# Kernel optimization log

Measured on AMD Instinct MI355X. Metric: run time of the kernel, lower is better.

## Reference

```python
import jax, jax.numpy as jnp
import numpy as np

N, E, HID, H_SA, H_MHA, L = 20000, 320000, 128, 4, 4, 32
MLP_HID = 4 * HID
EPS = 1e-6


def _ln(x, eps=EPS):
    mu = jnp.mean(x, axis=-1, keepdims=True)
    var = jnp.var(x, axis=-1, keepdims=True)
    return (x - mu) * jax.lax.rsqrt(var + eps)


def _modulate(x, shift, scale):
    return x * (1.0 + scale) + shift


def setup_inputs() -> dict:
    key = jax.random.key(0)
    ks = jax.random.split(key, 32)
    s = 0.02
    inp = {
        'x': jax.random.normal(ks[0], (N, HID), jnp.float32),
        'edge_index': jax.random.randint(ks[1], (2, E), 0, N, jnp.int64),
        't': jax.random.normal(ks[2], (N, HID), jnp.float32),
        'text_emb': jax.random.normal(ks[3], (N, L, HID), jnp.float32),
        # TransformerConv (per-head out_channels = HID, concat=False)
        'sa_q_w': jax.random.normal(ks[4], (HID, H_SA * HID), jnp.float32) * s,
        'sa_q_b': jnp.zeros((H_SA * HID,), jnp.float32),
        'sa_k_w': jax.random.normal(ks[5], (HID, H_SA * HID), jnp.float32) * s,
        'sa_k_b': jnp.zeros((H_SA * HID,), jnp.float32),
        'sa_v_w': jax.random.normal(ks[6], (HID, H_SA * HID), jnp.float32) * s,
        'sa_v_b': jnp.zeros((H_SA * HID,), jnp.float32),
        'sa_skip_w': jax.random.normal(ks[7], (HID, HID), jnp.float32) * s,
        'sa_skip_b': jnp.zeros((HID,), jnp.float32),
        # norm3 affine
        'n3_g': jnp.ones((HID,), jnp.float32),
        'n3_b': jnp.zeros((HID,), jnp.float32),
        # MultiheadAttention
        'mha_q_w': jax.random.normal(ks[8], (HID, HID), jnp.float32) * s,
        'mha_q_b': jnp.zeros((HID,), jnp.float32),
        'mha_k_w': jax.random.normal(ks[9], (HID, HID), jnp.float32) * s,
        'mha_k_b': jnp.zeros((HID,), jnp.float32),
        'mha_v_w': jax.random.normal(ks[10], (HID, HID), jnp.float32) * s,
        'mha_v_b': jnp.zeros((HID,), jnp.float32),
        'mha_o_w': jax.random.normal(ks[11], (HID, HID), jnp.float32) * s,
        'mha_o_b': jnp.zeros((HID,), jnp.float32),
        # MLP
        'fc1_w': jax.random.normal(ks[12], (HID, MLP_HID), jnp.float32) * s,
        'fc1_b': jnp.zeros((MLP_HID,), jnp.float32),
        'fc2_w': jax.random.normal(ks[13], (MLP_HID, HID), jnp.float32) * s,
        'fc2_b': jnp.zeros((HID,), jnp.float32),
        # adaLN modulation
        'ada_w': jax.random.normal(ks[14], (HID, 6 * HID), jnp.float32) * s,
        'ada_b': jnp.zeros((6 * HID,), jnp.float32),
    }
    return inp


def reference(x, edge_index, t, text_emb,
              sa_q_w, sa_q_b, sa_k_w, sa_k_b, sa_v_w, sa_v_b, sa_skip_w, sa_skip_b,
              n3_g, n3_b,
              mha_q_w, mha_q_b, mha_k_w, mha_k_b, mha_v_w, mha_v_b, mha_o_w, mha_o_b,
              fc1_w, fc1_b, fc2_w, fc2_b, ada_w, ada_b):
    n = x.shape[0]
    # adaLN: SiLU -> Linear -> chunk(6)
    mod = jax.nn.silu(t) @ ada_w + ada_b  # [N, 6*HID]
    shift_msa, scale_msa, gate_msa, shift_mlp, scale_mlp, gate_mlp = jnp.split(mod, 6, axis=1)

    # ---- graph self-attention (PyG TransformerConv, concat=False) ----
    xm = _modulate(_ln(x), shift_msa, scale_msa)  # [N, HID]
    q = (xm @ sa_q_w + sa_q_b).reshape(n, H_SA, HID)
    k = (xm @ sa_k_w + sa_k_b).reshape(n, H_SA, HID)
    v = (xm @ sa_v_w + sa_v_b).reshape(n, H_SA, HID)
    src, dst = edge_index[0], edge_index[1]  # messages flow src -> dst
    # per-edge attention logits [E, H]
    logits = jnp.einsum('ehd,ehd->eh', q[dst], k[src]) / jnp.sqrt(jnp.float32(HID))
    m = jax.ops.segment_max(logits, dst, num_segments=n)          # [N, H]
    ex = jnp.exp(logits - m[dst])                                  # [E, H]
    den = jax.ops.segment_sum(ex, dst, num_segments=n)            # [N, H]
    alpha = ex / den[dst]                                          # [E, H]
    agg = jax.ops.segment_sum(alpha[:, :, None] * v[src], dst, num_segments=n)  # [N, H, HID]
    sa_out = agg.mean(axis=1) + (xm @ sa_skip_w + sa_skip_b)       # concat=False -> head mean, + root skip
    x = x + gate_msa * sa_out

    # ---- cross attention: each node attends over its text memory ----
    qn = _ln(x) * n3_g + n3_b                                      # norm3 (affine)
    dh = HID // H_MHA
    qh = (qn @ mha_q_w + mha_q_b).reshape(n, H_MHA, dh)
    kh = (text_emb @ mha_k_w + mha_k_b).reshape(n, L, H_MHA, dh)
    vh = (text_emb @ mha_v_w + mha_v_b).reshape(n, L, H_MHA, dh)
    scores = jnp.einsum('nhd,nlhd->nhl', qh, kh) / jnp.sqrt(jnp.float32(dh))
    attn = jax.nn.softmax(scores, axis=-1)
    ctx = jnp.einsum('nhl,nlhd->nhd', attn, vh).reshape(n, HID)
    x = x + (ctx @ mha_o_w + mha_o_b)

    # ---- gated MLP ----
    xm2 = _modulate(_ln(x), shift_mlp, scale_mlp)
    h = jax.nn.gelu(xm2 @ fc1_w + fc1_b, approximate=True)
    x = x + gate_mlp * (h @ fc2_w + fc2_b)
    return x
```

## Files before the change

### kernel.cpp

```cpp
#include <hip/hip_runtime.h>
#include <hip/hip_bf16.h>
#include <math.h>

using ushort8 = __attribute__((ext_vector_type(8))) unsigned short;
using short8  = __attribute__((ext_vector_type(8))) short;
using f32x4   = __attribute__((ext_vector_type(4))) float;
using f32x2   = __attribute__((ext_vector_type(2))) float;

__device__ __forceinline__ float bf2f(unsigned short u) {
    union { unsigned int i; float f; } c; c.i = ((unsigned int)u) << 16; return c.f;
}
__device__ __forceinline__ unsigned short f2bf(float f) {
    __hip_bfloat16 h = __float2bfloat16(f);
    return *reinterpret_cast<unsigned short*>(&h);
}
__device__ __forceinline__ float silu_f(float x) { return x / (1.f + __expf(-x)); }
__device__ __forceinline__ float gelu_f(float x) {
    float x3 = x * x * x;
    return 0.5f * x * (1.f + tanhf(0.7978845608028654f * (x + 0.044715f * x3)));
}

constexpr int QKV_STRIDE_B = 2304;

template<int WM, int AIN, int PRE, int EPI, int OUTBF>
__global__ __launch_bounds__(256) void gemm_mfma(
    const void* __restrict__ Ain, const unsigned short* __restrict__ Wt,
    const float* __restrict__ bias, void* __restrict__ Cout,
    const float* __restrict__ res, const void* __restrict__ gatep,
    int Nrows, int K, int M)
{
    constexpr int BM = 32 * WM;
    __shared__ unsigned short As[BM][64];
    __shared__ unsigned short Bs[128][64];
    const int tid = threadIdx.x;
    const int row0 = blockIdx.x * BM;
    const int col0 = blockIdx.y * 128;
    const int lane = tid & 63;
    const int wid  = tid >> 6;
    const int wr = (wid >> 1) * 16 * WM;
    const int wc = (wid & 1) * 64;
    const int lr = lane & 15;
    const int lk = lane >> 4;

    f32x4 acc[WM][4];
#pragma unroll
    for (int i = 0; i < WM; i++)
#pragma unroll
        for (int j = 0; j < 4; j++) acc[i][j] = (f32x4)0.f;

    for (int k0 = 0; k0 < K; k0 += 64) {
#pragma unroll
        for (int i = 0; i < BM * 8 / 256; i++) {
            int f = tid + i * 256;
            int m = f >> 3, b = f & 7;
            int r = row0 + m;
            ushort8 h;
            if (r < Nrows) {
                if (AIN == 1) {
                    h = *(const ushort8*)((const unsigned short*)Ain + (size_t)r * K + k0 + b * 8);
                } else {
                    const float* ap = (const float*)Ain + (size_t)r * K + k0 + b * 8;
                    float4 p0 = *(const float4*)ap;
                    float4 p1 = *(const float4*)(ap + 4);
                    float v[8] = {p0.x, p0.y, p0.z, p0.w, p1.x, p1.y, p1.z, p1.w};
                    if (PRE == 1) {
#pragma unroll
                        for (int j = 0; j < 8; j++) v[j] = silu_f(v[j]);
                    }
#pragma unroll
                    for (int j = 0; j < 8; j++) h[j] = f2bf(v[j]);
                }
            } else {
#pragma unroll
                for (int j = 0; j < 8; j++) h[j] = 0;
            }
            *(ushort8*)&As[m][((b ^ (m & 7))) * 8] = h;
        }
#pragma unroll
        for (int i = 0; i < 4; i++) {
            int f = tid + i * 256;
            int n = f >> 3, b = f & 7;
            ushort8 w = *(const ushort8*)(Wt + (size_t)(col0 + n) * K + k0 + b * 8);
            *(ushort8*)&Bs[n][((b ^ (n & 7))) * 8] = w;
        }
        __syncthreads();

        short8 afr[WM][2], bfr[4][2];
#pragma unroll
        for (int fr = 0; fr < WM; fr++)
#pragma unroll
            for (int s = 0; s < 2; s++) {
                int m = wr + fr * 16 + lr;
                int blk = (s * 4 + lk) ^ (m & 7);
                afr[fr][s] = *(const short8*)&As[m][blk * 8];
            }
#pragma unroll
        for (int fc = 0; fc < 4; fc++)
#pragma unroll
            for (int s = 0; s < 2; s++) {
                int n = wc + fc * 16 + lr;
                int blk = (s * 4 + lk) ^ (n & 7);
                bfr[fc][s] = *(const short8*)&Bs[n][blk * 8];
            }
#pragma unroll
        for (int fr = 0; fr < WM; fr++)
#pragma unroll
            for (int fc = 0; fc < 4; fc++)
#pragma unroll
                for (int s = 0; s < 2; s++)
                    acc[fr][fc] = __builtin_amdgcn_mfma_f32_16x16x32_bf16(
                        afr[fr][s], bfr[fc][s], acc[fr][fc], 0, 0, 0);
        __syncthreads();
    }

#pragma unroll
    for (int fr = 0; fr < WM; fr++) {
#pragma unroll
        for (int fc = 0; fc < 4; fc++) {
#pragma unroll
            for (int r = 0; r < 4; r++) {
                int row = row0 + wr + fr * 16 + (lane >> 4) * 4 + r;
                if (row >= Nrows) continue;
                int col = col0 + wc + fc * 16 + (lane & 15);
                float val = acc[fr][fc][r] + bias[col];
                if (EPI == 4) {
                    unsigned char* rowp = (unsigned char*)Cout + (size_t)row * QKV_STRIDE_B;
                    if (col < 512) {
                        *(unsigned short*)(rowp + 2 * col) = f2bf(val);
                    } else if (col < 1536) {
                        int p = __builtin_amdgcn_cvt_pk_fp8_f32(val, 0.f, 0, false);
                        rowp[1024 + (col - 512)] = (unsigned char)(p & 0xff);
                    } else {
                        *(unsigned short*)(rowp + 2048 + 2 * (col - 1536)) = f2bf(val);
                    }
                } else {
                    size_t idx = (size_t)row * M + col;
                    if (EPI == 1) val = gelu_f(val);
                    else if (EPI == 2) val = res[idx] + val;
                    else if (EPI == 3) val = res[idx] +
                        bf2f(((const unsigned short*)gatep)[(size_t)row * 768 + col]) * val;
                    if (OUTBF) ((unsigned short*)Cout)[idx] = f2bf(val);
                    else       ((float*)Cout)[idx] = val;
                }
            }
        }
    }
}

__global__ __launch_bounds__(256) void conv_all(
    const float* __restrict__ qW, const float* __restrict__ qB,
    const float* __restrict__ kW, const float* __restrict__ kB,
    const float* __restrict__ vW, const float* __restrict__ vB,
    const float* __restrict__ sW, const float* __restrict__ sB,
    const float* __restrict__ f1W, const float* __restrict__ f2W,
    const float* __restrict__ adW,
    unsigned short* __restrict__ Wsa_t, float* __restrict__ bsa,
    unsigned short* __restrict__ fc1_t, unsigned short* __restrict__ fc2_t,
    unsigned short* __restrict__ ada_t)
{
    int g = blockIdx.x * 256 + threadIdx.x;
    if (g < 65536) {
        int m = g >> 7, kk = g & 127;
        Wsa_t[m * 128 + kk] = f2bf(qW[(size_t)kk * 512 + m]);
        if (kk == 0) bsa[m] = qB[m];
    } else if (g < 131072) {
        int l = g - 65536; int m = l >> 7, kk = l & 127;
        int p = 512 + ((m >> 2) << 3) + (m & 3);
        Wsa_t[p * 128 + kk] = f2bf(kW[(size_t)kk * 512 + m]);
        if (kk == 0) bsa[p] = kB[m];
    } else if (g < 196608) {
        int l = g - 131072; int m = l >> 7, kk = l & 127;
        int p = 516 + ((m >> 2) << 3) + (m & 3);
        Wsa_t[p * 128 + kk] = f2bf(vW[(size_t)kk * 512 + m]);
        if (kk == 0) bsa[p] = vB[m];
    } else if (g < 212992) {
        int l = g - 196608; int m = l >> 7, kk = l & 127;
        Wsa_t[(1536 + m) * 128 + kk] = f2bf(sW[(size_t)kk * 128 + m]);
        if (kk == 0) bsa[1536 + m] = sB[m];
    } else if (g < 278528) {
        int l = g - 212992; int m = l >> 7, kk = l & 127;
        fc1_t[m * 128 + kk] = f2bf(f1W[(size_t)kk * 512 + m]);
    } else if (g < 344064) {
        int l = g - 278528; int m = l >> 9, kk = l & 511;
        fc2_t[m * 512 + kk] = f2bf(f2W[(size_t)kk * 128 + m]);
    } else if (g < 442368) {
        int l = g - 344064; int m = l >> 7, kk = l & 127;
        ada_t[m * 128 + kk] = f2bf(adW[(size_t)kk * 768 + m]);
    }
}

__global__ __launch_bounds__(256) void prep_weights(
    const float* __restrict__ Wq, const float* __restrict__ bq,
    const float* __restrict__ Wk, const float* __restrict__ Wv,
    const float* __restrict__ bv, const float* __restrict__ Wo,
    const float* __restrict__ bo,
    unsigned short* __restrict__ Mcat_t, float* __restrict__ biasM,
    unsigned short* __restrict__ Pcat_t, float* __restrict__ co)
{
    int g = blockIdx.x * 256 + threadIdx.x;
    {
        int i0 = g >> 9, col = g & 511, h = col >> 7, i = col & 127;
        float s = 0.f;
#pragma unroll 8
        for (int j = 0; j < 32; j++)
            s += Wq[i0 * 128 + h * 32 + j] * Wk[i * 128 + h * 32 + j];
        Mcat_t[col * 128 + i0] = f2bf(s);
    }
    {
        int rowp = g >> 7, j = g & 127, h = rowp >> 7, i = rowp & 127;
        float s = 0.f;
#pragma unroll 8
        for (int d = 0; d < 32; d++)
            s += Wv[i * 128 + h * 32 + d] * Wo[(h * 32 + d) * 128 + j];
        Pcat_t[j * 512 + rowp] = f2bf(s);
    }
    if (g < 512) {
        int h = g >> 7, i = g & 127;
        float s = 0.f;
        for (int j = 0; j < 32; j++)
            s += bq[h * 32 + j] * Wk[i * 128 + h * 32 + j];
        biasM[g] = s;
    }
    if (g < 128) {
        float s = bo[g];
        for (int m = 0; m < 128; m++) s += bv[m] * Wo[m * 128 + g];
        co[g] = s;
    }
}

__global__ __launch_bounds__(256) void ln_mod_kernel(
    const float* __restrict__ x, const unsigned short* __restrict__ mod,
    int shift_off, int scale_off, unsigned short* __restrict__ outb, int N)
{
    int node = blockIdx.x * 4 + (threadIdx.x >> 6);
    if (node >= N) return;
    int lane = threadIdx.x & 63;
    f32x2 v = *(const f32x2*)(x + (size_t)node * 128 + lane * 2);
    float s = v[0] + v[1], ss = v[0] * v[0] + v[1] * v[1];
#pragma unroll
    for (int m = 1; m < 64; m <<= 1) { s += __shfl_xor(s, m); ss += __shfl_xor(ss, m); }
    float mu = s * (1.f / 128.f);
    float rs = rsqrtf(ss * (1.f / 128.f) - mu * mu + 1e-6f);
    const unsigned short* mp = mod + (size_t)node * 768;
    ushort2 sh = *(const ushort2*)(mp + shift_off + lane * 2);
    ushort2 sc = *(const ushort2*)(mp + scale_off + lane * 2);
    ushort2 o;
    o.x = f2bf((v[0] - mu) * rs * (1.f + bf2f(sc.x)) + bf2f(sh.x));
    o.y = f2bf((v[1] - mu) * rs * (1.f + bf2f(sc.y)) + bf2f(sh.y));
    *(ushort2*)(outb + (size_t)node * 128 + lane * 2) = o;
}

__global__ void count_edges(const int* __restrict__ dst, int* __restrict__ count, int E) {
    int e = blockIdx.x * blockDim.x + threadIdx.x;
    if (e < E) atomicAdd(&count[dst[e]], 1);
}

__global__ __launch_bounds__(1024) void scan_block(const int* __restrict__ cnt,
                                                   int* __restrict__ pre,
                                                   int* __restrict__ bsum, int n)
{
    __shared__ int tmp[1024];
    int gid = blockIdx.x * 1024 + threadIdx.x;
    int v = (gid < n) ? cnt[gid] : 0;
    tmp[threadIdx.x] = v;
    __syncthreads();
    for (int off = 1; off < 1024; off <<= 1) {
        int add = (threadIdx.x >= off) ? tmp[threadIdx.x - off] : 0;
        __syncthreads();
        tmp[threadIdx.x] += add;
        __syncthreads();
    }
    if (gid < n) pre[gid] = tmp[threadIdx.x];
    if (threadIdx.x == 1023) bsum[blockIdx.x] = tmp[1023];
}

__global__ void scan_tops(int* __restrict__ bsum, int nb) {
    if (threadIdx.x == 0 && blockIdx.x == 0) {
        int c = 0;
        for (int i = 0; i < nb; i++) { int v = bsum[i]; bsum[i] = c; c += v; }
    }
}

__global__ void scan_fix(const int* __restrict__ pre, const int* __restrict__ bsum,
                         const int* __restrict__ cnt,
                         int* __restrict__ base, int* __restrict__ cursor, int n)
{
    int gid = blockIdx.x * 256 + threadIdx.x;
    if (gid < n) {
        int inc = pre[gid] + bsum[gid >> 10];
        base[gid + 1] = inc;
        cursor[gid] = inc - cnt[gid];
    }
    if (gid == 0) base[0] = 0;
}

__global__ void scatter_edges(const int* __restrict__ src, const int* __restrict__ dst,
                              int* __restrict__ cursor, int* __restrict__ csr_src, int E) {
    int e = blockIdx.x * blockDim.x + threadIdx.x;
    if (e < E) {
        int pos = atomicAdd(&cursor[dst[e]], 1);
        csr_src[pos] = src[e];
    }
}

__global__ __launch_bounds__(128) void sa_node_kernel(
    const unsigned char* __restrict__ qkv,
    const int* __restrict__ base, const int* __restrict__ csr_src,
    const float* __restrict__ x, const unsigned short* __restrict__ mod,
    const float* __restrict__ n3g, const float* __restrict__ n3b,
    float* __restrict__ x1, unsigned short* __restrict__ qn)
{
    int node = blockIdx.x, t = threadIdx.x;
    const unsigned char* nrow = qkv + (size_t)node * QKV_STRIDE_B;
    ushort4 qu = *(const ushort4*)((const unsigned short*)nrow + t * 4);
    const float sc = 0.08838834764831845f;
    float q0 = bf2f(qu.x) * sc, q1 = bf2f(qu.y) * sc;
    float q2 = bf2f(qu.z) * sc, q3 = bf2f(qu.w) * sc;
    int beg = base[node], end = base[node + 1];
    float den = 0.f, a0 = 0.f, a1 = 0.f, a2 = 0.f, a3 = 0.f;
    uint2 kva = make_uint2(0, 0), kvb = make_uint2(0, 0);
    if (beg < end)
        kva = *(const uint2*)(qkv + (size_t)csr_src[beg] * QKV_STRIDE_B + 1024 + t * 8);
    if (beg + 1 < end)
        kvb = *(const uint2*)(qkv + (size_t)csr_src[beg + 1] * QKV_STRIDE_B + 1024 + t * 8);
    for (int e = beg; e < end; e++) {
        uint2 cur = kva;
        kva = kvb;
        if (e + 2 < end)
            kvb = *(const uint2*)(qkv + (size_t)csr_src[e + 2] * QKV_STRIDE_B + 1024 + t * 8);
        f32x2 k01 = __builtin_amdgcn_cvt_pk_f32_fp8(cur.x, false);
        f32x2 k23 = __builtin_amdgcn_cvt_pk_f32_fp8(cur.x, true);
        f32x2 v01 = __builtin_amdgcn_cvt_pk_f32_fp8(cur.y, false);
        f32x2 v23 = __builtin_amdgcn_cvt_pk_f32_fp8(cur.y, true);
        float p = q0 * k01[0] + q1 * k01[1] + q2 * k23[0] + q3 * k23[1];
#pragma unroll
        for (int mm = 1; mm < 32; mm <<= 1) p += __shfl_xor(p, mm);
        float pe = __expf(fminf(p, 80.f));
        den += pe;
        a0 += pe * v01[0];
        a1 += pe * v01[1];
        a2 += pe * v23[0];
        a3 += pe * v23[1];
    }
    float inv = (den > 0.f) ? 0.25f / den : 0.f;
    __shared__ float red[512];
    *(float4*)&red[t * 4] = make_float4(a0 * inv, a1 * inv, a2 * inv, a3 * inv);
    __syncthreads();
    float sa = red[t] + red[128 + t] + red[256 + t] + red[384 + t];
    float sab = bf2f(*(const unsigned short*)(nrow + 2048 + 2 * t));
    float g = bf2f(mod[(size_t)node * 768 + 256 + t]);
    size_t idx = (size_t)node * 128 + t;
    float xv = x[idx] + g * (sa + sab);
    x1[idx] = xv;
    float s = xv, ssq = xv * xv;
#pragma unroll
    for (int m = 1; m < 64; m <<= 1) { s += __shfl_xor(s, m); ssq += __shfl_xor(ssq, m); }
    __shared__ float l_s[2], l_ss[2];
    int w = t >> 6;
    if ((t & 63) == 0) { l_s[w] = s; l_ss[w] = ssq; }
    __syncthreads();
    float S = l_s[0] + l_s[1], SS = l_ss[0] + l_ss[1];
    float mu = S * (1.f / 128.f);
    float rs = rsqrtf(SS * (1.f / 128.f) - mu * mu + 1e-6f);
    qn[idx] = f2bf((xv - mu) * rs * n3g[t] + n3b[t]);
}

__global__ __launch_bounds__(128) void cross_mid_kernel(
    const float* __restrict__ te, const unsigned short* __restrict__ qw,
    unsigned short* __restrict__ u)
{
    int node = blockIdx.x, t = threadIdx.x;
    __shared__ float tes[32 * 132];
    __shared__ float qws[512];
    __shared__ float attnL[128];
#pragma unroll
    for (int i = 0; i < 8; i++) {
        int f = t + i * 128;
        int l = f >> 5, ii = (f & 31) * 4;
        float4 val = *(const float4*)(te + (size_t)node * 4096 + l * 128 + ii);
        *(float4*)&tes[l * 132 + ii] = val;
    }
    {
        ushort4 qv = *(const ushort4*)(qw + (size_t)node * 512 + t * 4);
        qws[t * 4 + 0] = bf2f(qv.x);
        qws[t * 4 + 1] = bf2f(qv.y);
        qws[t * 4 + 2] = bf2f(qv.z);
        qws[t * 4 + 3] = bf2f(qv.w);
    }
    __syncthreads();

    int h = t >> 5, l = t & 31;
    float sc = 0.f;
#pragma unroll 8
    for (int i = 0; i < 128; i++) sc += tes[l * 132 + i] * qws[h * 128 + i];
    sc *= 0.17677669529663687f;
    float mx = sc;
#pragma unroll
    for (int mm = 1; mm < 32; mm <<= 1) mx = fmaxf(mx, __shfl_xor(mx, mm));
    float e = __expf(sc - mx);
    float ssum = e;
#pragma unroll
    for (int mm = 1; mm < 32; mm <<= 1) ssum += __shfl_xor(ssum, mm);
    attnL[t] = e / ssum;
    __syncthreads();

    int i0 = t & 31;
    float u0 = 0, u1 = 0, u2 = 0, u3 = 0;
#pragma unroll 4
    for (int ll = 0; ll < 32; ll++) {
        float a = attnL[h * 32 + ll];
        u0 += a * tes[ll * 132 + i0];
        u1 += a * tes[ll * 132 + i0 + 32];
        u2 += a * tes[ll * 132 + i0 + 64];
        u3 += a * tes[ll * 132 + i0 + 96];
    }
    size_t ub = (size_t)node * 512 + h * 128;
    u[ub + i0] = f2bf(u0);
    u[ub + i0 + 32] = f2bf(u1);
    u[ub + i0 + 64] = f2bf(u2);
    u[ub + i0 + 96] = f2bf(u3);
}

extern "C" void kernel_launch(void* const* d_in, const int* in_sizes, int n_in,
                              void* d_out, int out_size, void* d_ws, size_t ws_size,
                              hipStream_t stream)
{
    const int N = in_sizes[0] / 128;
    const int E = in_sizes[1] / 2;

    const float* x      = (const float*)d_in[0];
    const int*   ei     = (const int*)d_in[1];
    const float* t_in   = (const float*)d_in[2];
    const float* te     = (const float*)d_in[3];
    const float* sa_q_w = (const float*)d_in[4];
    const float* sa_q_b = (const float*)d_in[5];
    const float* sa_k_w = (const float*)d_in[6];
    const float* sa_k_b = (const float*)d_in[7];
    const float* sa_v_w = (const float*)d_in[8];
    const float* sa_v_b = (const float*)d_in[9];
    const float* sa_skip_w = (const float*)d_in[10];
    const float* sa_skip_b = (const float*)d_in[11];
    const float* n3_g   = (const float*)d_in[12];
    const float* n3_b   = (const float*)d_in[13];
    const float* mha_q_w = (const float*)d_in[14];
    const float* mha_q_b = (const float*)d_in[15];
    const float* mha_k_w = (const float*)d_in[16];
    const float* mha_v_w = (const float*)d_in[18];
    const float* mha_v_b = (const float*)d_in[19];
    const float* mha_o_w = (const float*)d_in[20];
    const float* mha_o_b = (const float*)d_in[21];
    const float* fc1_w  = (const float*)d_in[22];
    const float* fc1_b  = (const float*)d_in[23];
    const float* fc2_w  = (const float*)d_in[24];
    const float* fc2_b  = (const float*)d_in[25];
    const float* ada_w  = (const float*)d_in[26];
    const float* ada_b  = (const float*)d_in[27];
    float* out = (float*)d_out;

    float* ws = (float*)d_ws;
    size_t o = 0;
    unsigned short* modb = (unsigned short*)(ws + o); o += (size_t)N * 384;
    unsigned short* Bbuf = (unsigned short*)(ws + o); o += (size_t)N * 64;
    unsigned short* Qn   = (unsigned short*)(ws + o); o += (size_t)N * 64;
    unsigned short* Cbuf = (unsigned short*)(ws + o); o += (size_t)N * 256;
    unsigned short* Dbuf = (unsigned short*)(ws + o); o += (size_t)N * 256;
    unsigned short* Ebuf = (unsigned short*)(ws + o); o += (size_t)N * 256;
    float* Gbuf = ws + o; o += (size_t)N * 128;
    unsigned char* QKV = (unsigned char*)(ws + o); o += (size_t)N * (QKV_STRIDE_B / 4);
    unsigned short* Wsa_t  = (unsigned short*)(ws + o); o += 1664 * 128 / 2;
    unsigned short* Mcat_t = (unsigned short*)(ws + o); o += 512 * 128 / 2;
    unsigned short* Pcat_t = (unsigned short*)(ws + o); o += 128 * 512 / 2;
    unsigned short* fc1_t  = (unsigned short*)(ws + o); o += 512 * 128 / 2;
    unsigned short* fc2_t  = (unsigned short*)(ws + o); o += 128 * 512 / 2;
    unsigned short* ada_t  = (unsigned short*)(ws + o); o += 768 * 128 / 2;
    float* bsa   = ws + o; o += 1664;
    float* biasM = ws + o; o += 512;
    float* co    = ws + o; o += 128;
    int* count   = (int*)(ws + o); o += N;
    int* base    = (int*)(ws + o); o += N + 4;
    int* cursor  = (int*)(ws + o); o += N;
    int* pre     = (int*)(ws + o); o += N;
    int* bsum    = (int*)(ws + o); o += 32;
    int* csr_src = (int*)(ws + o); o += E;

    const int* src = ei;
    const int* dst = ei + E;
    const int rb128 = (N + 127) / 128;
    const int rb64  = (N + 63) / 64;
    const int nScan = (N + 1023) / 1024;

    conv_all<<<1728, 256, 0, stream>>>(sa_q_w, sa_q_b, sa_k_w, sa_k_b,
                                       sa_v_w, sa_v_b, sa_skip_w, sa_skip_b,
                                       fc1_w, fc2_w, ada_w,
                                       Wsa_t, bsa, fc1_t, fc2_t, ada_t);
    prep_weights<<<256, 256, 0, stream>>>(mha_q_w, mha_q_b, mha_k_w, mha_v_w,
                                          mha_v_b, mha_o_w, mha_o_b,
                                          Mcat_t, biasM, Pcat_t, co);

    hipMemsetAsync(count, 0, (size_t)N * sizeof(int), stream);
    count_edges<<<(E + 255) / 256, 256, 0, stream>>>(dst, count, E);
    scan_block<<<nScan, 1024, 0, stream>>>(count, pre, bsum, N);
    scan_tops<<<1, 64, 0, stream>>>(bsum, nScan);
    scan_fix<<<(N + 255) / 256, 256, 0, stream>>>(pre, bsum, count, base, cursor, N);
    scatter_edges<<<(E + 255) / 256, 256, 0, stream>>>(src, dst, cursor, csr_src, E);

    gemm_mfma<4, 0, 1, 0, 1><<<dim3(rb128, 6), 256, 0, stream>>>(
        t_in, ada_t, ada_b, modb, nullptr, nullptr, N, 128, 768);

    ln_mod_kernel<<<(N + 3) / 4, 256, 0, stream>>>(x, modb, 0, 128, Bbuf, N);

    gemm_mfma<4, 1, 0, 4, 1><<<dim3(rb128, 13), 256, 0, stream>>>(
        Bbuf, Wsa_t, bsa, QKV, nullptr, nullptr, N, 128, 1664);

    sa_node_kernel<<<N, 128, 0, stream>>>(QKV, base, csr_src, x, modb,
                                          n3_g, n3_b, Gbuf, Qn);

    gemm_mfma<4, 1, 0, 0, 1><<<dim3(rb128, 4), 256, 0, stream>>>(
        Qn, Mcat_t, biasM, Cbuf, nullptr, nullptr, N, 128, 512);
    cross_mid_kernel<<<N, 128, 0, stream>>>(te, Cbuf, Dbuf);
    gemm_mfma<2, 1, 0, 2, 0><<<dim3(rb64, 1), 256, 0, stream>>>(
        Dbuf, Pcat_t, co, Gbuf, Gbuf, nullptr, N, 512, 128);

    ln_mod_kernel<<<(N + 3) / 4, 256, 0, stream>>>(Gbuf, modb, 384, 512, Bbuf, N);
    gemm_mfma<4, 1, 0, 1, 1><<<dim3(rb128, 4), 256, 0, stream>>>(
        Bbuf, fc1_t, fc1_b, Ebuf, nullptr, nullptr, N, 128, 512);
    gemm_mfma<2, 1, 0, 3, 0><<<dim3(rb64, 1), 256, 0, stream>>>(
        Ebuf, fc2_t, fc2_b, out, Gbuf, modb + 640, N, 512, 128);
}
```

Before: 382.6 us.

## Fuse LayerNorm-modulate into K=128 GEMMs with single-stage full-K tiles

Adds a KF=1 GEMM path that loads the whole K=128 slab into shared memory in one pass. In PRE=2 mode it computes LayerNorm plus adaLN shift/scale inside the A-tile load, which removes the two ln_mod_kernel launches and their bf16 round-trip buffer. The SA edge loop is also unrolled by two, with dual accumulators and deeper prefetch. The cost is a larger LDS footprint for these GEMMs and redundant LN statistics recomputed by every column block (13 blocks for QKV, 4 for fc1).

```diff
diff --git a/kernel.cpp b/kernel.cpp
--- a/kernel.cpp
+++ b/kernel.cpp
@@ -22,16 +22,18 @@
 
 constexpr int QKV_STRIDE_B = 2304;
 
-template<int WM, int AIN, int PRE, int EPI, int OUTBF>
+template<int WM, int KF, int AIN, int PRE, int EPI, int OUTBF>
 __global__ __launch_bounds__(256) void gemm_mfma(
     const void* __restrict__ Ain, const unsigned short* __restrict__ Wt,
     const float* __restrict__ bias, void* __restrict__ Cout,
     const float* __restrict__ res, const void* __restrict__ gatep,
+    const unsigned short* __restrict__ mod, int shift_off, int scale_off,
     int Nrows, int K, int M)
 {
     constexpr int BM = 32 * WM;
-    __shared__ unsigned short As[BM][64];
-    __shared__ unsigned short Bs[128][64];
+    constexpr int KW = KF ? 128 : 64;
+    __shared__ unsigned short As[BM][KW];
+    __shared__ unsigned short Bs[128][KW];
     const int tid = threadIdx.x;
     const int row0 = blockIdx.x * BM;
     const int col0 = blockIdx.y * 128;
@@ -48,18 +50,55 @@
 #pragma unroll
         for (int j = 0; j < 4; j++) acc[i][j] = (f32x4)0.f;
 
-    for (int k0 = 0; k0 < K; k0 += 64) {
-#pragma unroll
-        for (int i = 0; i < BM * 8 / 256; i++) {
+    if (KF == 1) {
+#pragma unroll
+        for (int i = 0; i < BM * 16 / 256; i++) {
             int f = tid + i * 256;
-            int m = f >> 3, b = f & 7;
+            int m = f >> 4, b = f & 15;
             int r = row0 + m;
             ushort8 h;
-            if (r < Nrows) {
-                if (AIN == 1) {
-                    h = *(const ushort8*)((const unsigned short*)Ain + (size_t)r * K + k0 + b * 8);
+            if (PRE == 2) {
+                float v[8];
+                if (r < Nrows) {
+                    const float* ap = (const float*)Ain + (size_t)r * 128 + b * 8;
+                    float4 p0 = *(const float4*)ap;
+                    float4 p1 = *(const float4*)(ap + 4);
+                    v[0]=p0.x; v[1]=p0.y; v[2]=p0.z; v[3]=p0.w;
+                    v[4]=p1.x; v[5]=p1.y; v[6]=p1.z; v[7]=p1.w;
                 } else {
-                    const float* ap = (const float*)Ain + (size_t)r * K + k0 + b * 8;
+#pragma unroll
+                    for (int j = 0; j < 8; j++) v[j] = 0.f;
+                }
+                float s = 0.f, ss = 0.f;
+#pragma unroll
+                for (int j = 0; j < 8; j++) { s += v[j]; ss += v[j] * v[j]; }
+#pragma unroll
+                for (int mm = 1; mm < 16; mm <<= 1) {
+                    s += __shfl_xor(s, mm); ss += __shfl_xor(ss, mm);
+                }
+                float mu = s * (1.f / 128.f);
+                float rs = rsqrtf(ss * (1.f / 128.f) - mu * mu + 1e-6f);
+                if (r < Nrows) {
+                    const unsigned short* mp = mod + (size_t)r * 768;
+                    ushort8 shv = *(const ushort8*)(mp + shift_off + b * 8);
+                    ushort8 scv = *(const ushort8*)(mp + scale_off + b * 8);
+#pragma unroll
+                    for (int j = 0; j < 8; j++)
+                        h[j] = f2bf((v[j] - mu) * rs * (1.f + bf2f(scv[j])) + bf2f(shv[j]));
+                } else {
+#pragma unroll
+                    for (int j = 0; j < 8; j++) h[j] = 0;
+                }
+            } else if (AIN == 1) {
+                if (r < Nrows)
+                    h = *(const ushort8*)((const unsigned short*)Ain + (size_t)r * 128 + b * 8);
+                else {
+#pragma unroll
+                    for (int j = 0; j < 8; j++) h[j] = 0;
+                }
+            } else {
+                if (r < Nrows) {
+                    const float* ap = (const float*)Ain + (size_t)r * 128 + b * 8;
                     float4 p0 = *(const float4*)ap;
                     float4 p1 = *(const float4*)(ap + 4);
                     float v[8] = {p0.x, p0.y, p0.z, p0.w, p1.x, p1.y, p1.z, p1.w};
@@ -69,48 +108,95 @@
                     }
 #pragma unroll
                     for (int j = 0; j < 8; j++) h[j] = f2bf(v[j]);
-                }
-            } else {
-#pragma unroll
-                for (int j = 0; j < 8; j++) h[j] = 0;
+                } else {
+#pragma unroll
+                    for (int j = 0; j < 8; j++) h[j] = 0;
+                }
             }
             *(ushort8*)&As[m][((b ^ (m & 7))) * 8] = h;
         }
 #pragma unroll
-        for (int i = 0; i < 4; i++) {
+        for (int i = 0; i < 8; i++) {
             int f = tid + i * 256;
-            int n = f >> 3, b = f & 7;
-            ushort8 w = *(const ushort8*)(Wt + (size_t)(col0 + n) * K + k0 + b * 8);
+            int n = f >> 4, b = f & 15;
+            ushort8 w = *(const ushort8*)(Wt + (size_t)(col0 + n) * 128 + b * 8);
             *(ushort8*)&Bs[n][((b ^ (n & 7))) * 8] = w;
         }
         __syncthreads();
-
-        short8 afr[WM][2], bfr[4][2];
-#pragma unroll
-        for (int fr = 0; fr < WM; fr++)
-#pragma unroll
-            for (int s = 0; s < 2; s++) {
+#pragma unroll
+        for (int s = 0; s < 4; s++) {
+            short8 afr[WM], bfr[4];
+#pragma unroll
+            for (int fr = 0; fr < WM; fr++) {
                 int m = wr + fr * 16 + lr;
                 int blk = (s * 4 + lk) ^ (m & 7);
-                afr[fr][s] = *(const short8*)&As[m][blk * 8];
+                afr[fr] = *(const short8*)&As[m][blk * 8];
             }
 #pragma unroll
-        for (int fc = 0; fc < 4; fc++)
-#pragma unroll
-            for (int s = 0; s < 2; s++) {
+            for (int fc = 0; fc < 4; fc++) {
                 int n = wc + fc * 16 + lr;
                 int blk = (s * 4 + lk) ^ (n & 7);
-                bfr[fc][s] = *(const short8*)&Bs[n][blk * 8];
+                bfr[fc] = *(const short8*)&Bs[n][blk * 8];
             }
 #pragma unroll
-        for (int fr = 0; fr < WM; fr++)
+            for (int fr = 0; fr < WM; fr++)
+#pragma unroll
+                for (int fc = 0; fc < 4; fc++)
+                    acc[fr][fc] = __builtin_amdgcn_mfma_f32_16x16x32_bf16(
+                        afr[fr], bfr[fc], acc[fr][fc], 0, 0, 0);
+        }
+    } else {
+        for (int k0 = 0; k0 < K; k0 += 64) {
+#pragma unroll
+            for (int i = 0; i < BM * 8 / 256; i++) {
+                int f = tid + i * 256;
+                int m = f >> 3, b = f & 7;
+                int r = row0 + m;
+                ushort8 h;
+                if (r < Nrows) {
+                    h = *(const ushort8*)((const unsigned short*)Ain + (size_t)r * K + k0 + b * 8);
+                } else {
+#pragma unroll
+                    for (int j = 0; j < 8; j++) h[j] = 0;
+                }
+                *(ushort8*)&As[m][((b ^ (m & 7))) * 8] = h;
+            }
+#pragma unroll
+            for (int i = 0; i < 4; i++) {
+                int f = tid + i * 256;
+                int n = f >> 3, b = f & 7;
+                ushort8 w = *(const ushort8*)(Wt + (size_t)(col0 + n) * K + k0 + b * 8);
+                *(ushort8*)&Bs[n][((b ^ (n & 7))) * 8] = w;
+            }
+            __syncthreads();
+
+            short8 afr[WM][2], bfr[4][2];
+#pragma unroll
+            for (int fr = 0; fr < WM; fr++)
+#pragma unroll
+                for (int s = 0; s < 2; s++) {
+                    int m = wr + fr * 16 + lr;
+                    int blk = (s * 4 + lk) ^ (m & 7);
+                    afr[fr][s] = *(const short8*)&As[m][blk * 8];
+                }
 #pragma unroll
             for (int fc = 0; fc < 4; fc++)
 #pragma unroll
-                for (int s = 0; s < 2; s++)
-                    acc[fr][fc] = __builtin_amdgcn_mfma_f32_16x16x32_bf16(
-                        afr[fr][s], bfr[fc][s], acc[fr][fc], 0, 0, 0);
-        __syncthreads();
+                for (int s = 0; s < 2; s++) {
+                    int n = wc + fc * 16 + lr;
+                    int blk = (s * 4 + lk) ^ (n & 7);
+                    bfr[fc][s] = *(const short8*)&Bs[n][blk * 8];
+                }
+#pragma unroll
+            for (int fr = 0; fr < WM; fr++)
+#pragma unroll
+                for (int fc = 0; fc < 4; fc++)
+#pragma unroll
+                    for (int s = 0; s < 2; s++)
+                        acc[fr][fc] = __builtin_amdgcn_mfma_f32_16x16x32_bf16(
+                            afr[fr][s], bfr[fc][s], acc[fr][fc], 0, 0, 0);
+            __syncthreads();
+        }
     }
 
 #pragma unroll
@@ -228,28 +314,6 @@
     }
 }
 
-__global__ __launch_bounds__(256) void ln_mod_kernel(
-    const float* __restrict__ x, const unsigned short* __restrict__ mod,
-    int shift_off, int scale_off, unsigned short* __restrict__ outb, int N)
-{
-    int node = blockIdx.x * 4 + (threadIdx.x >> 6);
-    if (node >= N) return;
-    int lane = threadIdx.x & 63;
-    f32x2 v = *(const f32x2*)(x + (size_t)node * 128 + lane * 2);
-    float s = v[0] + v[1], ss = v[0] * v[0] + v[1] * v[1];
-#pragma unroll
-    for (int m = 1; m < 64; m <<= 1) { s += __shfl_xor(s, m); ss += __shfl_xor(ss, m); }
-    float mu = s * (1.f / 128.f);
-    float rs = rsqrtf(ss * (1.f / 128.f) - mu * mu + 1e-6f);
-    const unsigned short* mp = mod + (size_t)node * 768;
-    ushort2 sh = *(const ushort2*)(mp + shift_off + lane * 2);
-    ushort2 sc = *(const ushort2*)(mp + scale_off + lane * 2);
-    ushort2 o;
-    o.x = f2bf((v[0] - mu) * rs * (1.f + bf2f(sc.x)) + bf2f(sh.x));
-    o.y = f2bf((v[1] - mu) * rs * (1.f + bf2f(sc.y)) + bf2f(sh.y));
-    *(ushort2*)(outb + (size_t)node * 128 + lane * 2) = o;
-}
-
 __global__ void count_edges(const int* __restrict__ dst, int* __restrict__ count, int E) {
     int e = blockIdx.x * blockDim.x + threadIdx.x;
     if (e < E) atomicAdd(&count[dst[e]], 1);
@@ -317,31 +381,45 @@
     float q0 = bf2f(qu.x) * sc, q1 = bf2f(qu.y) * sc;
     float q2 = bf2f(qu.z) * sc, q3 = bf2f(qu.w) * sc;
     int beg = base[node], end = base[node + 1];
-    float den = 0.f, a0 = 0.f, a1 = 0.f, a2 = 0.f, a3 = 0.f;
-    uint2 kva = make_uint2(0, 0), kvb = make_uint2(0, 0);
+    float den0 = 0.f, a00 = 0.f, a01 = 0.f, a02 = 0.f, a03 = 0.f;
+    float den1 = 0.f, a10 = 0.f, a11 = 0.f, a12 = 0.f, a13 = 0.f;
+    uint2 c0 = make_uint2(0, 0), c1 = make_uint2(0, 0);
     if (beg < end)
-        kva = *(const uint2*)(qkv + (size_t)csr_src[beg] * QKV_STRIDE_B + 1024 + t * 8);
+        c0 = *(const uint2*)(qkv + (size_t)csr_src[beg] * QKV_STRIDE_B + 1024 + t * 8);
     if (beg + 1 < end)
-        kvb = *(const uint2*)(qkv + (size_t)csr_src[beg + 1] * QKV_STRIDE_B + 1024 + t * 8);
-    for (int e = beg; e < end; e++) {
-        uint2 cur = kva;
-        kva = kvb;
+        c1 = *(const uint2*)(qkv + (size_t)csr_src[beg + 1] * QKV_STRIDE_B + 1024 + t * 8);
+    for (int e = beg; e < end; e += 2) {
+        uint2 m0 = c0, m1 = c1;
         if (e + 2 < end)
-            kvb = *(const uint2*)(qkv + (size_t)csr_src[e + 2] * QKV_STRIDE_B + 1024 + t * 8);
-        f32x2 k01 = __builtin_amdgcn_cvt_pk_f32_fp8(cur.x, false);
-        f32x2 k23 = __builtin_amdgcn_cvt_pk_f32_fp8(cur.x, true);
-        f32x2 v01 = __builtin_amdgcn_cvt_pk_f32_fp8(cur.y, false);
-        f32x2 v23 = __builtin_amdgcn_cvt_pk_f32_fp8(cur.y, true);
-        float p = q0 * k01[0] + q1 * k01[1] + q2 * k23[0] + q3 * k23[1];
-#pragma unroll
-        for (int mm = 1; mm < 32; mm <<= 1) p += __shfl_xor(p, mm);
-        float pe = __expf(fminf(p, 80.f));
-        den += pe;
-        a0 += pe * v01[0];
-        a1 += pe * v01[1];
-        a2 += pe * v23[0];
-        a3 += pe * v23[1];
-    }
+            c0 = *(const uint2*)(qkv + (size_t)csr_src[e + 2] * QKV_STRIDE_B + 1024 + t * 8);
+        if (e + 3 < end)
+            c1 = *(const uint2*)(qkv + (size_t)csr_src[e + 3] * QKV_STRIDE_B + 1024 + t * 8);
+        f32x2 k01 = __builtin_amdgcn_cvt_pk_f32_fp8(m0.x, false);
+        f32x2 k23 = __builtin_amdgcn_cvt_pk_f32_fp8(m0.x, true);
+        f32x2 l01 = __builtin_amdgcn_cvt_pk_f32_fp8(m1.x, false);
+        f32x2 l23 = __builtin_amdgcn_cvt_pk_f32_fp8(m1.x, true);
+        float p0 = q0 * k01[0] + q1 * k01[1] + q2 * k23[0] + q3 * k23[1];
+        float p1 = q0 * l01[0] + q1 * l01[1] + q2 * l23[0] + q3 * l23[1];
+#pragma unroll
+        for (int mm = 1; mm < 32; mm <<= 1) {
+            p0 += __shfl_xor(p0, mm);
+            p1 += __shfl_xor(p1, mm);
+        }
+        float pe0 = __expf(fminf(p0, 80.f));
+        float pe1 = (e + 1 < end) ? __expf(fminf(p1, 80.f)) : 0.f;
+        f32x2 v01 = __builtin_amdgcn_cvt_pk_f32_fp8(m0.y, false);
+        f32x2 v23 = __builtin_amdgcn_cvt_pk_f32_fp8(m0.y, true);
+        f32x2 w01 = __builtin_amdgcn_cvt_pk_f32_fp8(m1.y, false);
+        f32x2 w23 = __builtin_amdgcn_cvt_pk_f32_fp8(m1.y, true);
+        den0 += pe0;
+        a00 += pe0 * v01[0]; a01 += pe0 * v01[1];
+        a02 += pe0 * v23[0]; a03 += pe0 * v23[1];
+        den1 += pe1;
+        a10 += pe1 * w01[0]; a11 += pe1 * w01[1];
+        a12 += pe1 * w23[0]; a13 += pe1 * w23[1];
+    }
+    float den = den0 + den1;
+    float a0 = a00 + a10, a1 = a01 + a11, a2 = a02 + a12, a3 = a03 + a13;
     float inv = (den > 0.f) ? 0.25f / den : 0.f;
     __shared__ float red[512];
     *(float4*)&red[t * 4] = make_float4(a0 * inv, a1 * inv, a2 * inv, a3 * inv);
@@ -460,7 +538,6 @@
     float* ws = (float*)d_ws;
     size_t o = 0;
     unsigned short* modb = (unsigned short*)(ws + o); o += (size_t)N * 384;
-    unsigned short* Bbuf = (unsigned short*)(ws + o); o += (size_t)N * 64;
     unsigned short* Qn   = (unsigned short*)(ws + o); o += (size_t)N * 64;
     unsigned short* Cbuf = (unsigned short*)(ws + o); o += (size_t)N * 256;
     unsigned short* Dbuf = (unsigned short*)(ws + o); o += (size_t)N * 256;
@@ -504,26 +581,23 @@
     scan_fix<<<(N + 255) / 256, 256, 0, stream>>>(pre, bsum, count, base, cursor, N);
     scatter_edges<<<(E + 255) / 256, 256, 0, stream>>>(src, dst, cursor, csr_src, E);
 
-    gemm_mfma<4, 0, 1, 0, 1><<<dim3(rb128, 6), 256, 0, stream>>>(
-        t_in, ada_t, ada_b, modb, nullptr, nullptr, N, 128, 768);
-
-    ln_mod_kernel<<<(N + 3) / 4, 256, 0, stream>>>(x, modb, 0, 128, Bbuf, N);
-
-    gemm_mfma<4, 1, 0, 4, 1><<<dim3(rb128, 13), 256, 0, stream>>>(
-        Bbuf, Wsa_t, bsa, QKV, nullptr, nullptr, N, 128, 1664);
+    gemm_mfma<4, 1, 0, 1, 0, 1><<<dim3(rb128, 6), 256, 0, stream>>>(
+        t_in, ada_t, ada_b, modb, nullptr, nullptr, nullptr, 0, 0, N, 128, 768);
+
+    gemm_mfma<4, 1, 0, 2, 4, 1><<<dim3(rb128, 13), 256, 0, stream>>>(
+        x, Wsa_t, bsa, QKV, nullptr, nullptr, modb, 0, 128, N, 128, 1664);
 
     sa_node_kernel<<<N, 128, 0, stream>>>(QKV, base, csr_src, x, modb,
                                           n3_g, n3_b, Gbuf, Qn);
 
-    gemm_mfma<4, 1, 0, 0, 1><<<dim3(rb128, 4), 256, 0, stream>>>(
-        Qn, Mcat_t, biasM, Cbuf, nullptr, nullptr, N, 128, 512);
+    gemm_mfma<4, 1, 1, 0, 0, 1><<<dim3(rb128, 4), 256, 0, stream>>>(
+        Qn, Mcat_t, biasM, Cbuf, nullptr, nullptr, nullptr, 0, 0, N, 128, 512);
     cross_mid_kernel<<<N, 128, 0, stream>>>(te, Cbuf, Dbuf);
-    gemm_mfma<2, 1, 0, 2, 0><<<dim3(rb64, 1), 256, 0, stream>>>(
-        Dbuf, Pcat_t, co, Gbuf, Gbuf, nullptr, N, 512, 128);
-
-    ln_mod_kernel<<<(N + 3) / 4, 256, 0, stream>>>(Gbuf, modb, 384, 512, Bbuf, N);
-    gemm_mfma<4, 1, 0, 1, 1><<<dim3(rb128, 4), 256, 0, stream>>>(
-        Bbuf, fc1_t, fc1_b, Ebuf, nullptr, nullptr, N, 128, 512);
-    gemm_mfma<2, 1, 0, 3, 0><<<dim3(rb64, 1), 256, 0, stream>>>(
-        Ebuf, fc2_t, fc2_b, out, Gbuf, modb + 640, N, 512, 128);
-}
+    gemm_mfma<2, 0, 1, 0, 2, 0><<<dim3(rb64, 1), 256, 0, stream>>>(
+        Dbuf, Pcat_t, co, Gbuf, Gbuf, nullptr, nullptr, 0, 0, N, 512, 128);
+
+    gemm_mfma<4, 1, 0, 2, 1, 1><<<dim3(rb128, 4), 256, 0, stream>>>(
+        Gbuf, fc1_t, fc1_b, Ebuf, nullptr, nullptr, modb, 384, 512, N, 128, 512);
+    gemm_mfma<2, 0, 1, 0, 3, 0><<<dim3(rb64, 1), 256, 0, stream>>>(
+        Ebuf, fc2_t, fc2_b, out, Gbuf, modb + 640, nullptr, 0, 0, N, 512, 128);
+}
```

Result: slower. 436.8 us (+14.2%).

## Unroll graph-attention edge loop by four, merge weight prep kernels, vectorize score dot

Applied to the files above, without the earlier changes.

The per-node graph attention loop now processes four edges per iteration. It prefetches four neighbor K/V rows ahead and interleaves four independent shuffle reductions to expose more memory and ILP parallelism. The two weight-preparation kernels are merged into one launch to drop a kernel boundary. The cross-attention score dot product reads LDS with float4 loads. The unrolled loop raises register pressure and adds tail masking for degrees not divisible by four.

```diff
diff --git a/kernel.cpp b/kernel.cpp
--- a/kernel.cpp
+++ b/kernel.cpp
@@ -147,7 +147,7 @@
     }
 }
 
-__global__ __launch_bounds__(256) void conv_all(
+__global__ __launch_bounds__(256) void prep_all(
     const float* __restrict__ qW, const float* __restrict__ qB,
     const float* __restrict__ kW, const float* __restrict__ kB,
     const float* __restrict__ vW, const float* __restrict__ vB,
@@ -156,7 +156,13 @@
     const float* __restrict__ adW,
     unsigned short* __restrict__ Wsa_t, float* __restrict__ bsa,
     unsigned short* __restrict__ fc1_t, unsigned short* __restrict__ fc2_t,
-    unsigned short* __restrict__ ada_t)
+    unsigned short* __restrict__ ada_t,
+    const float* __restrict__ Wq, const float* __restrict__ bq,
+    const float* __restrict__ Wk, const float* __restrict__ Wv,
+    const float* __restrict__ bv, const float* __restrict__ Wo,
+    const float* __restrict__ bo,
+    unsigned short* __restrict__ Mcat_t, float* __restrict__ biasM,
+    unsigned short* __restrict__ Pcat_t, float* __restrict__ co)
 {
     int g = blockIdx.x * 256 + threadIdx.x;
     if (g < 65536) {
@@ -186,45 +192,36 @@
     } else if (g < 442368) {
         int l = g - 344064; int m = l >> 7, kk = l & 127;
         ada_t[m * 128 + kk] = f2bf(adW[(size_t)kk * 768 + m]);
-    }
-}
-
-__global__ __launch_bounds__(256) void prep_weights(
-    const float* __restrict__ Wq, const float* __restrict__ bq,
-    const float* __restrict__ Wk, const float* __restrict__ Wv,
-    const float* __restrict__ bv, const float* __restrict__ Wo,
-    const float* __restrict__ bo,
-    unsigned short* __restrict__ Mcat_t, float* __restrict__ biasM,
-    unsigned short* __restrict__ Pcat_t, float* __restrict__ co)
-{
-    int g = blockIdx.x * 256 + threadIdx.x;
-    {
-        int i0 = g >> 9, col = g & 511, h = col >> 7, i = col & 127;
-        float s = 0.f;
+    } else {
+        int g2 = g - 442368;
+        {
+            int i0 = g2 >> 9, col = g2 & 511, h = col >> 7, i = col & 127;
+            float s = 0.f;
 #pragma unroll 8
-        for (int j = 0; j < 32; j++)
-            s += Wq[i0 * 128 + h * 32 + j] * Wk[i * 128 + h * 32 + j];
-        Mcat_t[col * 128 + i0] = f2bf(s);
-    }
-    {
-        int rowp = g >> 7, j = g & 127, h = rowp >> 7, i = rowp & 127;
-        float s = 0.f;
+            for (int j = 0; j < 32; j++)
+                s += Wq[i0 * 128 + h * 32 + j] * Wk[i * 128 + h * 32 + j];
+            Mcat_t[col * 128 + i0] = f2bf(s);
+        }
+        {
+            int rowp = g2 >> 7, j = g2 & 127, h = rowp >> 7, i = rowp & 127;
+            float s = 0.f;
 #pragma unroll 8
-        for (int d = 0; d < 32; d++)
-            s += Wv[i * 128 + h * 32 + d] * Wo[(h * 32 + d) * 128 + j];
-        Pcat_t[j * 512 + rowp] = f2bf(s);
-    }
-    if (g < 512) {
-        int h = g >> 7, i = g & 127;
-        float s = 0.f;
-        for (int j = 0; j < 32; j++)
-            s += bq[h * 32 + j] * Wk[i * 128 + h * 32 + j];
-        biasM[g] = s;
-    }
-    if (g < 128) {
-        float s = bo[g];
-        for (int m = 0; m < 128; m++) s += bv[m] * Wo[m * 128 + g];
-        co[g] = s;
+            for (int d = 0; d < 32; d++)
+                s += Wv[i * 128 + h * 32 + d] * Wo[(h * 32 + d) * 128 + j];
+            Pcat_t[j * 512 + rowp] = f2bf(s);
+        }
+        if (g2 < 512) {
+            int h = g2 >> 7, i = g2 & 127;
+            float s = 0.f;
+            for (int j = 0; j < 32; j++)
+                s += bq[h * 32 + j] * Wk[i * 128 + h * 32 + j];
+            biasM[g2] = s;
+        }
+        if (g2 < 128) {
+            float s = bo[g2];
+            for (int m = 0; m < 128; m++) s += bv[m] * Wo[m * 128 + g2];
+            co[g2] = s;
+        }
     }
 }
 
@@ -313,35 +310,72 @@
     int node = blockIdx.x, t = threadIdx.x;
     const unsigned char* nrow = qkv + (size_t)node * QKV_STRIDE_B;
     ushort4 qu = *(const ushort4*)((const unsigned short*)nrow + t * 4);
-    const float sc = 0.08838834764831845f;
-    float q0 = bf2f(qu.x) * sc, q1 = bf2f(qu.y) * sc;
-    float q2 = bf2f(qu.z) * sc, q3 = bf2f(qu.w) * sc;
+    const float scl = 0.08838834764831845f;
+    float q0 = bf2f(qu.x) * scl, q1 = bf2f(qu.y) * scl;
+    float q2 = bf2f(qu.z) * scl, q3 = bf2f(qu.w) * scl;
     int beg = base[node], end = base[node + 1];
-    float den = 0.f, a0 = 0.f, a1 = 0.f, a2 = 0.f, a3 = 0.f;
-    uint2 kva = make_uint2(0, 0), kvb = make_uint2(0, 0);
+    float den = 0.f;
+    float a0 = 0.f, a1 = 0.f, a2 = 0.f, a3 = 0.f;
+    float b0 = 0.f, b1 = 0.f, b2 = 0.f, b3 = 0.f;
+    uint2 c0 = make_uint2(0, 0), c1 = c0, c2 = c0, c3 = c0;
     if (beg < end)
-        kva = *(const uint2*)(qkv + (size_t)csr_src[beg] * QKV_STRIDE_B + 1024 + t * 8);
+        c0 = *(const uint2*)(qkv + (size_t)csr_src[beg] * QKV_STRIDE_B + 1024 + t * 8);
     if (beg + 1 < end)
-        kvb = *(const uint2*)(qkv + (size_t)csr_src[beg + 1] * QKV_STRIDE_B + 1024 + t * 8);
-    for (int e = beg; e < end; e++) {
-        uint2 cur = kva;
-        kva = kvb;
-        if (e + 2 < end)
-            kvb = *(const uint2*)(qkv + (size_t)csr_src[e + 2] * QKV_STRIDE_B + 1024 + t * 8);
-        f32x2 k01 = __builtin_amdgcn_cvt_pk_f32_fp8(cur.x, false);
-        f32x2 k23 = __builtin_amdgcn_cvt_pk_f32_fp8(cur.x, true);
-        f32x2 v01 = __builtin_amdgcn_cvt_pk_f32_fp8(cur.y, false);
-        f32x2 v23 = __builtin_amdgcn_cvt_pk_f32_fp8(cur.y, true);
-        float p = q0 * k01[0] + q1 * k01[1] + q2 * k23[0] + q3 * k23[1];
-#pragma unroll
-        for (int mm = 1; mm < 32; mm <<= 1) p += __shfl_xor(p, mm);
-        float pe = __expf(fminf(p, 80.f));
-        den += pe;
-        a0 += pe * v01[0];
-        a1 += pe * v01[1];
-        a2 += pe * v23[0];
-        a3 += pe * v23[1];
-    }
+        c1 = *(const uint2*)(qkv + (size_t)csr_src[beg + 1] * QKV_STRIDE_B + 1024 + t * 8);
+    if (beg + 2 < end)
+        c2 = *(const uint2*)(qkv + (size_t)csr_src[beg + 2] * QKV_STRIDE_B + 1024 + t * 8);
+    if (beg + 3 < end)
+        c3 = *(const uint2*)(qkv + (size_t)csr_src[beg + 3] * QKV_STRIDE_B + 1024 + t * 8);
+    for (int e = beg; e < end; e += 4) {
+        uint2 m0 = c0, m1 = c1, m2 = c2, m3 = c3;
+        if (e + 4 < end)
+            c0 = *(const uint2*)(qkv + (size_t)csr_src[e + 4] * QKV_STRIDE_B + 1024 + t * 8);
+        if (e + 5 < end)
+            c1 = *(const uint2*)(qkv + (size_t)csr_src[e + 5] * QKV_STRIDE_B + 1024 + t * 8);
+        if (e + 6 < end)
+            c2 = *(const uint2*)(qkv + (size_t)csr_src[e + 6] * QKV_STRIDE_B + 1024 + t * 8);
+        if (e + 7 < end)
+            c3 = *(const uint2*)(qkv + (size_t)csr_src[e + 7] * QKV_STRIDE_B + 1024 + t * 8);
+        f32x2 k01, k23;
+        k01 = __builtin_amdgcn_cvt_pk_f32_fp8(m0.x, false);
+        k23 = __builtin_amdgcn_cvt_pk_f32_fp8(m0.x, true);
+        float p0 = q0 * k01[0] + q1 * k01[1] + q2 * k23[0] + q3 * k23[1];
+        k01 = __builtin_amdgcn_cvt_pk_f32_fp8(m1.x, false);
+        k23 = __builtin_amdgcn_cvt_pk_f32_fp8(m1.x, true);
+        float p1 = q0 * k01[0] + q1 * k01[1] + q2 * k23[0] + q3 * k23[1];
+        k01 = __builtin_amdgcn_cvt_pk_f32_fp8(m2.x, false);
+        k23 = __builtin_amdgcn_cvt_pk_f32_fp8(m2.x, true);
+        float p2 = q0 * k01[0] + q1 * k01[1] + q2 * k23[0] + q3 * k23[1];
+        k01 = __builtin_amdgcn_cvt_pk_f32_fp8(m3.x, false);
+        k23 = __builtin_amdgcn_cvt_pk_f32_fp8(m3.x, true);
+        float p3 = q0 * k01[0] + q1 * k01[1] + q2 * k23[0] + q3 * k23[1];
+#pragma unroll
+        for (int mm = 1; mm < 32; mm <<= 1) {
+            p0 += __shfl_xor(p0, mm);
+            p1 += __shfl_xor(p1, mm);
+            p2 += __shfl_xor(p2, mm);
+            p3 += __shfl_xor(p3, mm);
+        }
+        float pe0 = __expf(fminf(p0, 80.f));
+        float pe1 = (e + 1 < end) ? __expf(fminf(p1, 80.f)) : 0.f;
+        float pe2 = (e + 2 < end) ? __expf(fminf(p2, 80.f)) : 0.f;
+        float pe3 = (e + 3 < end) ? __expf(fminf(p3, 80.f)) : 0.f;
+        den += (pe0 + pe1) + (pe2 + pe3);
+        f32x2 v01, v23;
+        v01 = __builtin_amdgcn_cvt_pk_f32_fp8(m0.y, false);
+        v23 = __builtin_amdgcn_cvt_pk_f32_fp8(m0.y, true);
+        a0 += pe0 * v01[0]; a1 += pe0 * v01[1]; a2 += pe0 * v23[0]; a3 += pe0 * v23[1];
+        v01 = __builtin_amdgcn_cvt_pk_f32_fp8(m1.y, false);
+        v23 = __builtin_amdgcn_cvt_pk_f32_fp8(m1.y, true);
+        b0 += pe1 * v01[0]; b1 += pe1 * v01[1]; b2 += pe1 * v23[0]; b3 += pe1 * v23[1];
+        v01 = __builtin_amdgcn_cvt_pk_f32_fp8(m2.y, false);
+        v23 = __builtin_amdgcn_cvt_pk_f32_fp8(m2.y, true);
+        a0 += pe2 * v01[0]; a1 += pe2 * v01[1]; a2 += pe2 * v23[0]; a3 += pe2 * v23[1];
+        v01 = __builtin_amdgcn_cvt_pk_f32_fp8(m3.y, false);
+        v23 = __builtin_amdgcn_cvt_pk_f32_fp8(m3.y, true);
+        b0 += pe3 * v01[0]; b1 += pe3 * v01[1]; b2 += pe3 * v23[0]; b3 += pe3 * v23[1];
+    }
+    a0 += b0; a1 += b1; a2 += b2; a3 += b3;
     float inv = (den > 0.f) ? 0.25f / den : 0.f;
     __shared__ float red[512];
     *(float4*)&red[t * 4] = make_float4(a0 * inv, a1 * inv, a2 * inv, a3 * inv);
@@ -391,8 +425,12 @@
 
     int h = t >> 5, l = t & 31;
     float sc = 0.f;
-#pragma unroll 8
-    for (int i = 0; i < 128; i++) sc += tes[l * 132 + i] * qws[h * 128 + i];
+#pragma unroll
+    for (int i = 0; i < 32; i++) {
+        float4 tv = *(const float4*)&tes[l * 132 + i * 4];
+        float4 qv4 = *(const float4*)&qws[h * 128 + i * 4];
+        sc += tv.x * qv4.x + tv.y * qv4.y + tv.z * qv4.z + tv.w * qv4.w;
+    }
     sc *= 0.17677669529663687f;
     float mx = sc;
 #pragma unroll
@@ -489,13 +527,13 @@
     const int rb64  = (N + 63) / 64;
     const int nScan = (N + 1023) / 1024;
 
-    conv_all<<<1728, 256, 0, stream>>>(sa_q_w, sa_q_b, sa_k_w, sa_k_b,
+    prep_all<<<1984, 256, 0, stream>>>(sa_q_w, sa_q_b, sa_k_w, sa_k_b,
                                        sa_v_w, sa_v_b, sa_skip_w, sa_skip_b,
                                        fc1_w, fc2_w, ada_w,
-                                       Wsa_t, bsa, fc1_t, fc2_t, ada_t);
-    prep_weights<<<256, 256, 0, stream>>>(mha_q_w, mha_q_b, mha_k_w, mha_v_w,
-                                          mha_v_b, mha_o_w, mha_o_b,
-                                          Mcat_t, biasM, Pcat_t, co);
+                                       Wsa_t, bsa, fc1_t, fc2_t, ada_t,
+                                       mha_q_w, mha_q_b, mha_k_w, mha_v_w,
+                                       mha_v_b, mha_o_w, mha_o_b,
+                                       Mcat_t, biasM, Pcat_t, co);
 
     hipMemsetAsync(count, 0, (size_t)N * sizeof(int), stream);
     count_edges<<<(E + 255) / 256, 256, 0, stream>>>(dst, count, E);
```

After: 378.6 us. Within noise of the previous version (-1.0%).
